# Kernel tuning notes

Measured on AMD Instinct MI355X. Metric: run time of the kernel, lower is better.

The kernel has to match this reference:

```python
import jax, jax.numpy as jnp
import numpy as np

BS, L = 4096, 20
NF, EF, TF = 128, 128, 128
DM = 3 * NF + EF + TF          # 640: attention model dim
DIN = DM - TF                  # 512: GRU input dim
NHEAD = 2
NNODES, NEDGES = 100000, 500000
ODE_STEPS = 8


def setup_inputs() -> dict:
    key = jax.random.key(0)
    ks = jax.random.split(key, 32)
    p = lambda i, shape, s: jax.random.normal(ks[i], shape, dtype=jnp.float32) * s
    return {
        'nids': jax.random.randint(ks[0], (BS,), 1, NNODES),
        'ts': jax.random.uniform(ks[1], (BS,), dtype=jnp.float32),
        'hist_nids': jax.random.randint(ks[2], (BS, L), 0, NNODES),
        'anonymized_ids': jax.random.randint(ks[3], (BS, L), 0, L + 1),
        'hist_eids': jax.random.randint(ks[4], (BS, L), 0, NEDGES),
        'hist_ts': jnp.sort(jax.random.uniform(ks[5], (BS, L), dtype=jnp.float32), axis=1),
        'hist_dirs': jax.random.randint(ks[6], (BS, L), 0, 2),
        'node_feat': p(7, (NNODES, NF), 0.1),
        'edge_feat': p(8, (NEDGES, EF), 0.1),
        'anony_emb': p(9, (L + 1, NF), 0.1),
        'time_w': p(10, (TF,), 1.0),
        'time_b': p(11, (TF,), 1.0),
        'in_proj_w': p(12, (3 * DM, DM), 0.02),
        'in_proj_b': jnp.zeros((3 * DM,), jnp.float32),
        'out_proj_w': p(13, (DM, DM), 0.02),
        'out_proj_b': jnp.zeros((DM,), jnp.float32),
        'outfn_w': p(14, (NF, DM), 0.02),
        'outfn_b': jnp.zeros((NF,), jnp.float32),
        'attn_wq': p(15, (NF, NF), 0.05),
        'attn_wk': p(16, (NF + EF + TF, NF), 0.05),
        'attn_wv': p(17, (NF + EF + TF, NF), 0.05),
        'merge_w': p(18, (2 * NF, NF), 0.05),
        'merge_b': jnp.zeros((NF,), jnp.float32),
        'gru_w_ih': p(19, (3 * NF, DIN), 0.05),
        'gru_w_hh': p(20, (3 * NF, NF), 0.05),
        'gru_b_ih': jnp.zeros((3 * NF,), jnp.float32),
        'gru_b_hh': jnp.zeros((3 * NF,), jnp.float32),
        'ode_w': p(21, (NF, NF), 0.05),
        'ode_b': jnp.zeros((NF,), jnp.float32),
        'tnode_w': p(22, (NF,), 1.0),
        'tnode_b': p(23, (NF,), 1.0),
    }


def reference(nids, ts, hist_nids, anonymized_ids, hist_eids, hist_ts, hist_dirs,
              node_feat, edge_feat, anony_emb, time_w, time_b,
              in_proj_w, in_proj_b, out_proj_w, out_proj_b, outfn_w, outfn_b,
              attn_wq, attn_wk, attn_wv, merge_w, merge_b,
              gru_w_ih, gru_w_hh, gru_b_ih, gru_b_hh,
              ode_w, ode_b, tnode_w, tnode_b):
    bs, hl = hist_nids.shape
    mask = (hist_nids == 0)
    mask = mask.at[:, -1].set(False)
    invalid_rows = jnp.all(mask, axis=1, keepdims=True)  # [bs,1]

    r_nids = jnp.broadcast_to(nids[:, None], (bs, hl))
    src_nids = r_nids * hist_dirs + hist_nids * (1 - hist_dirs)
    dst_nids = r_nids * (1 - hist_dirs) + hist_nids * hist_dirs

    src_vals = node_feat[src_nids]                 # [bs,L,NF] gather
    dst_vals = node_feat[dst_nids]                 # [bs,L,NF] gather
    edge_vals = edge_feat[hist_eids]               # [bs,L,EF] gather
    anony_vals = anony_emb[anonymized_ids]         # [bs,L,NF] gather
    dt = hist_ts[:, -1:] - hist_ts                 # [bs,L]
    ts_vals = jnp.cos(dt[..., None] * time_w + time_b)  # [bs,L,TF] TimeEncode

    full_vals = jnp.concatenate([src_vals, dst_vals, anony_vals, edge_vals, ts_vals], axis=2)
    last_event_feat = full_vals[:, -1, :DIN]
    full_vals = full_vals.at[:, -1, :DIN].set(0.0)

    # --- self MHA over history (nn.MultiheadAttention with key_padding_mask) ---
    qkv = full_vals @ in_proj_w.T + in_proj_b      # [bs,L,3*DM]
    q, k, v = jnp.split(qkv, 3, axis=-1)
    dh = DM // NHEAD
    rs = lambda x: x.reshape(bs, hl, NHEAD, dh)
    scores = jnp.einsum('blhd,bmhd->bhlm', rs(q), rs(k)) / np.sqrt(dh)
    scores = jnp.where(mask[:, None, None, :], -1e9, scores)
    attn = jax.nn.softmax(scores, axis=-1)
    ctx = jnp.einsum('bhlm,bmhd->blhd', attn, rs(v)).reshape(bs, hl, DM)
    mha_out = ctx @ out_proj_w.T + out_proj_b

    # --- temporal graph attention embedding (GraphAttnEmbedding stand-in) ---
    qn = mha_out[:, -1] @ outfn_w.T + outfn_b      # [bs,NF]
    nb = jnp.concatenate([node_feat[hist_nids], edge_vals, ts_vals], axis=2)  # [bs,L,NF+EF+TF]
    qh = qn @ attn_wq                              # [bs,NF]
    kh = nb @ attn_wk                              # [bs,L,NF]
    vh = nb @ attn_wv                              # [bs,L,NF]
    sc = jnp.einsum('bd,bld->bl', qh, kh) / np.sqrt(NF)
    sc = jnp.where(mask, -1e9, sc)
    a = jax.nn.softmax(sc, axis=-1)
    ctx2 = jnp.einsum('bl,bld->bd', a, vh)
    h_prev_left = jnp.tanh(jnp.concatenate([ctx2, node_feat[nids]], axis=1) @ merge_w + merge_b)

    # --- GRUCell jump update ---
    gi = last_event_feat @ gru_w_ih.T + gru_b_ih
    gh = h_prev_left @ gru_w_hh.T + gru_b_hh
    ir, iz, inn = jnp.split(gi, 3, axis=-1)
    hr, hz, hn = jnp.split(gh, 3, axis=-1)
    r = jax.nn.sigmoid(ir + hr)
    zg = jax.nn.sigmoid(iz + hz)
    n = jnp.tanh(inn + r * hn)
    h_prev_right = (1.0 - zg) * n + zg * h_prev_left

    # --- neural ODE transform (RK4 over s in [0,1]) ---
    t0 = hist_ts[:, -2:-1]                         # prev_prev_ts [bs,1]
    t1 = hist_ts[:, -1:]                           # prev_ts      [bs,1]
    ratio = t1 - t0                                # (end-start)=1.0

    def f(s, z):
        t = s * ratio + t0                         # [bs,1]
        te = jnp.cos(t * tnode_w + tnode_b)        # [bs,NF]
        return jnp.tanh((z + te) @ ode_w.T + ode_b) * ratio

    ds = 1.0 / ODE_STEPS

    def step(z, s):
        k1 = f(s, z)
        k2 = f(s + 0.5 * ds, z + 0.5 * ds * k1)
        k3 = f(s + 0.5 * ds, z + 0.5 * ds * k2)
        k4 = f(s + ds, z + ds * k3)
        return z + (ds / 6.0) * (k1 + 2 * k2 + 2 * k3 + k4), None

    h_left, _ = jax.lax.scan(step, h_prev_right, jnp.arange(ODE_STEPS, dtype=jnp.float32) * ds)

    h_left = jnp.where(invalid_rows, 0.0, h_left)
    h_right = jnp.where(invalid_rows, 0.0, h_prev_right)
    return h_left, h_right, hist_ts[:, -1]
```

## Files before the change

kernel.cpp:

```cpp
#include <hip/hip_runtime.h>
#include <math.h>

#define BSZ 4096
#define HL  20
#define NF  128
#define DM  640
#define DIN 512
#define DH  320

static __device__ __forceinline__ float sigmoidf_(float x){ return 1.f/(1.f+expf(-x)); }
static __device__ __forceinline__ unsigned short f2b_(float v){
    return (unsigned short)((__float_as_uint(v) + 0x8000u) >> 16);
}
static __device__ __forceinline__ float b2f_(unsigned short u){
    return __uint_as_float(((unsigned int)u) << 16);
}

__global__ void k_comb(const float* __restrict__ outfn_w,
                       const float* __restrict__ out_proj_w,
                       float* __restrict__ combT)
{
    int jc = blockIdx.x, jq = threadIdx.x;
    float acc = 0.f;
    for (int e = 0; e < DM; ++e)
        acc += outfn_w[jq*DM + e] * out_proj_w[e*DM + jc];
    combT[jc*NF + jq] = acc;
}

__global__ void k_zz(const float* __restrict__ in_proj_w,
                     const float* __restrict__ combT,
                     float* __restrict__ ZZ)
{
    int ef = blockIdx.x;
    int h = ef / DM, e = ef - h*DM;
    int jq = threadIdx.x;
    const float* wv = in_proj_w + (2*DM + h*DH)*DM + e;
    const float* cb = combT + (h*DH)*NF + jq;
    float acc = 0.f;
    for (int dd = 0; dd < DH; ++dd)
        acc += wv[dd*DM] * cb[dd*NF];
    ZZ[ef*NF + jq] = acc;
}

__global__ void k_qbias(const float* __restrict__ outfn_b,
                        const float* __restrict__ out_proj_b,
                        const float* __restrict__ outfn_w,
                        const float* __restrict__ in_proj_b,
                        const float* __restrict__ combT,
                        float* __restrict__ qb)
{
    int jq = threadIdx.x;
    float acc = outfn_b[jq];
    for (int e = 0; e < DM; ++e)  acc += out_proj_b[e] * outfn_w[jq*DM + e];
    for (int jc = 0; jc < DM; ++jc) acc += in_proj_b[2*DM + jc] * combT[jc*NF + jq];
    qb[jq] = acc;
}

__global__ void k_transpose(const float* __restrict__ gih,
                            const float* __restrict__ ghh,
                            float* __restrict__ giT,
                            float* __restrict__ ghT)
{
    int i = blockIdx.x*blockDim.x + threadIdx.x;
    if (i < DIN*3*NF) {
        int d = i / (3*NF), j = i - d*(3*NF);
        giT[i] = gih[j*DIN + d];
    } else {
        int i2 = i - DIN*3*NF;
        int d = i2 / (3*NF), j = i2 - d*(3*NF);
        ghT[i2] = ghh[j*NF + d];
    }
}

__global__ void k_qc(const float* __restrict__ time_b,
                     const float* __restrict__ in_proj_w,
                     const float* __restrict__ in_proj_b,
                     float* __restrict__ qcv)
{
    __shared__ float tsr[NF];
    int tid = threadIdx.x;
    tsr[tid] = cosf(time_b[tid]);
    __syncthreads();
    int j = blockIdx.x*128 + tid;
    const float* wr = in_proj_w + j*DM + DIN;
    float acc = in_proj_b[j];
    for (int d = 0; d < NF; ++d) acc += tsr[d]*wr[d];
    qcv[j] = acc;
}

__global__ void k_cc(const float* __restrict__ qcv,
                     const float* __restrict__ in_proj_b,
                     float* __restrict__ cc)
{
    int wave = threadIdx.x >> 6, lane = threadIdx.x & 63;
    float acc = 0.f;
    for (int j = lane; j < DH; j += 64)
        acc += qcv[wave*DH + j] * in_proj_b[DM + wave*DH + j];
    for (int off = 32; off > 0; off >>= 1) acc += __shfl_down(acc, off);
    if (lane == 0) cc[wave] = acc;
}

__global__ void k_u(const float* __restrict__ qcv,
                    const float* __restrict__ in_proj_w,
                    float* __restrict__ u)
{
    int d = blockIdx.x*64 + threadIdx.x;
    int h = d / DM, dd = d - h*DM;
    const float* base = in_proj_w + (DM + h*DH)*DM + dd;
    const float* q = qcv + h*DH;
    float acc = 0.f;
    for (int j = 0; j < DH; ++j) acc += q[j]*base[j*DM];
    u[d] = acc;
}

__global__ __launch_bounds__(256) void k_attn1(
    const int* __restrict__ nids, const int* __restrict__ hist_nids,
    const int* __restrict__ aidsp, const int* __restrict__ eidsp,
    const float* __restrict__ hist_ts, const int* __restrict__ dirsp,
    const float* __restrict__ node_feat, const float* __restrict__ edge_feat,
    const float* __restrict__ anony_emb,
    const float* __restrict__ time_w, const float* __restrict__ time_b,
    const float* __restrict__ u, const float* __restrict__ cc,
    float* __restrict__ wbuf, float* __restrict__ lef)
{
    int b = blockIdx.x, tid = threadIdx.x;
    int wave = tid >> 6, lane = tid & 63;
    __shared__ unsigned short zh[HL][DM];
    __shared__ float ul[2*DM];
    __shared__ float sc[2][HL];
    __shared__ float aw[2][HL];
    __shared__ int   shn[HL], sdir[HL], said[HL], seid[HL];
    __shared__ float sts[HL];

    if (tid < HL) {
        shn[tid]  = hist_nids[b*HL+tid];
        sdir[tid] = dirsp[b*HL+tid];
        said[tid] = aidsp[b*HL+tid];
        seid[tid] = eidsp[b*HL+tid];
        sts[tid]  = hist_ts[b*HL+tid];
    }
    for (int i = tid; i < 2*DM; i += 256) ul[i] = u[i];
    float twA = time_w[lane],    tbA = time_b[lane];
    float twB = time_w[64+lane], tbB = time_b[64+lane];
    __syncthreads();

    float ulr0[10], ulr1[10];
    #pragma unroll
    for (int s = 0; s < 10; ++s) {
        ulr0[s] = ul[s*64 + lane];
        ulr1[s] = ul[DM + s*64 + lane];
    }

    int rnid = nids[b];
    float tlast = sts[HL-1];

    int srcv[5], dstv[5], aidv[5], eidv[5];
    float dtv[5];
    #pragma unroll
    for (int r = 0; r < 5; ++r) {
        int l = wave + 4*r;
        int hn = shn[l], dir = sdir[l];
        srcv[r] = dir ? rnid : hn;
        dstv[r] = dir ? hn : rnid;
        aidv[r] = said[l];
        eidv[r] = eidv[r] = seid[l];
        dtv[r]  = tlast - sts[l];
    }
    float zr[5][10];
    #pragma unroll
    for (int r = 0; r < 5; ++r) {
        zr[r][0] = node_feat[srcv[r]*NF + lane];
        zr[r][1] = node_feat[srcv[r]*NF + 64 + lane];
        zr[r][2] = node_feat[dstv[r]*NF + lane];
        zr[r][3] = node_feat[dstv[r]*NF + 64 + lane];
        zr[r][4] = anony_emb[aidv[r]*NF + lane];
        zr[r][5] = anony_emb[aidv[r]*NF + 64 + lane];
        zr[r][6] = edge_feat[eidv[r]*NF + lane];
        zr[r][7] = edge_feat[eidv[r]*NF + 64 + lane];
        zr[r][8] = cosf(dtv[r]*twA + tbA);
        zr[r][9] = cosf(dtv[r]*twB + tbB);
    }
    float c0 = cc[0], c1 = cc[1];
    #pragma unroll
    for (int r = 0; r < 5; ++r) {
        int l = wave + 4*r;
        if (l == HL-1) {
            #pragma unroll
            for (int s = 0; s < 8; ++s) {
                lef[b*DIN + s*64 + lane] = zr[r][s];
                zr[r][s] = 0.f;
            }
        }
        float d0 = 0.f, d1 = 0.f;
        #pragma unroll
        for (int s = 0; s < 10; ++s) {
            float v = zr[r][s];
            d0 += ulr0[s]*v;
            d1 += ulr1[s]*v;
            zh[l][s*64 + lane] = f2b_(v);
        }
        for (int off = 32; off > 0; off >>= 1) {
            d0 += __shfl_down(d0, off);
            d1 += __shfl_down(d1, off);
        }
        if (lane == 0) {
            bool msk = (shn[l] == 0) && (l != HL-1);
            sc[0][l] = msk ? -1.0e9f : (d0 + c0)*0.05590169943749474f;
            sc[1][l] = msk ? -1.0e9f : (d1 + c1)*0.05590169943749474f;
        }
    }
    __syncthreads();
    if (tid < 2) {
        float mx = -3.0e38f;
        for (int m = 0; m < HL; ++m) mx = fmaxf(mx, sc[tid][m]);
        float sum = 0.f;
        for (int m = 0; m < HL; ++m) { float e = expf(sc[tid][m]-mx); aw[tid][m] = e; sum += e; }
        float inv = 1.f/sum;
        for (int m = 0; m < HL; ++m) aw[tid][m] *= inv;
    }
    __syncthreads();
    #pragma unroll
    for (int i = tid; i < 2*DM; i += 256) {
        int h = i / DM, d = i - h*DM;
        float acc = 0.f;
        #pragma unroll
        for (int m = 0; m < HL; ++m) acc += aw[h][m]*b2f_(zh[m][d]);
        wbuf[b*2*DM + i] = acc;
    }
}

__global__ __launch_bounds__(256) void k_gemm_qn(const float* __restrict__ A,
                                                 const float* __restrict__ BT,
                                                 const float* __restrict__ bias,
                                                 float* __restrict__ C)
{
    constexpr int K = 2*DM;
    __shared__ float As[8*K];
    int r0 = blockIdx.x*8, tid = threadIdx.x;
    for (int i = tid; i < 8*K; i += 256) As[i] = A[r0*K + i];
    __syncthreads();
    int j = tid & (NF-1), rh = tid >> 7;
    const float* bp = BT + j;
    const float* ap = As + rh*4*K;
    float acc0=0.f, acc1=0.f, acc2=0.f, acc3=0.f;
    for (int d = 0; d < K; ++d) {
        float bv = bp[d*NF];
        acc0 += ap[d]*bv;
        acc1 += ap[K + d]*bv;
        acc2 += ap[2*K + d]*bv;
        acc3 += ap[3*K + d]*bv;
    }
    float bsv = bias[j];
    int rb = r0 + rh*4;
    C[(rb+0)*NF + j] = acc0 + bsv;
    C[(rb+1)*NF + j] = acc1 + bsv;
    C[(rb+2)*NF + j] = acc2 + bsv;
    C[(rb+3)*NF + j] = acc3 + bsv;
}

__global__ __launch_bounds__(256) void k_gemm_gi(const float* __restrict__ A,
                                                 const float* __restrict__ BT,
                                                 const float* __restrict__ bias,
                                                 float* __restrict__ C)
{
    constexpr int K = DIN;
    constexpr int N = 3*NF;
    __shared__ float As[8*K];
    int r0 = blockIdx.x*8, tid = threadIdx.x;
    for (int i = tid; i < 8*K; i += 256) As[i] = A[r0*K + i];
    __syncthreads();
    int j0 = tid, j1 = tid + 256;
    bool has1 = (j1 < N);
    float a0[8] = {0,0,0,0,0,0,0,0};
    float a1[8] = {0,0,0,0,0,0,0,0};
    for (int d = 0; d < K; ++d) {
        float b0 = BT[d*N + j0];
        float b1 = 0.f;
        if (has1) b1 = BT[d*N + j1];
        #pragma unroll
        for (int r = 0; r < 8; ++r) {
            float av = As[r*K + d];
            a0[r] += av*b0;
            a1[r] += av*b1;
        }
    }
    float bs0 = bias[j0];
    for (int r = 0; r < 8; ++r) C[(r0+r)*N + j0] = a0[r] + bs0;
    if (has1) {
        float bs1 = bias[j1];
        for (int r = 0; r < 8; ++r) C[(r0+r)*N + j1] = a1[r] + bs1;
    }
}

__global__ __launch_bounds__(128) void k_attn2(
    const int* __restrict__ nids, const int* __restrict__ hist_nids,
    const int* __restrict__ eidsp, const float* __restrict__ hist_ts,
    const float* __restrict__ node_feat, const float* __restrict__ edge_feat,
    const float* __restrict__ time_w, const float* __restrict__ time_b,
    const float* __restrict__ attn_wq, const float* __restrict__ attn_wk,
    const float* __restrict__ attn_wv,
    const float* __restrict__ merge_w, const float* __restrict__ merge_b,
    const float* __restrict__ qn, const float* __restrict__ gi,
    const float* __restrict__ ghT, const float* __restrict__ gru_b_hh,
    float* __restrict__ hpr_out, float* __restrict__ out)
{
    int b = blockIdx.x, tid = threadIdx.x;
    __shared__ float qns[NF], qh[NF], p[3*NF], nbar[3*NF];
    __shared__ float scl[HL], al[HL];
    __shared__ float ctx2[NF], hpl[NF], nfn[NF];
    __shared__ int   shn[HL], seid[HL];
    __shared__ float sts[HL];

    if (tid < HL) {
        shn[tid]  = hist_nids[b*HL+tid];
        seid[tid] = eidsp[b*HL+tid];
        sts[tid]  = hist_ts[b*HL+tid];
    }
    qns[tid] = qn[b*NF + tid];
    nfn[tid] = node_feat[nids[b]*NF + tid];
    __syncthreads();

    float tlast = sts[HL-1];
    {
        float acc = 0.f;
        for (int d = 0; d < NF; ++d) acc += qns[d]*attn_wq[d*NF + tid];
        qh[tid] = acc;
    }
    __syncthreads();
    for (int dd = tid; dd < 3*NF; dd += NF) {
        const float4* row4 = (const float4*)(attn_wk + dd*NF);
        float acc = 0.f;
        #pragma unroll
        for (int q4 = 0; q4 < NF/4; ++q4) {
            float4 w4 = row4[q4];
            acc += w4.x*qh[4*q4] + w4.y*qh[4*q4+1] + w4.z*qh[4*q4+2] + w4.w*qh[4*q4+3];
        }
        p[dd] = acc;
    }
    __syncthreads();
    int wave = tid >> 6, lane = tid & 63;
    for (int l = wave; l < HL; l += 2) {
        int hn = shn[l], eid = seid[l];
        float dt = tlast - sts[l];
        float acc = 0.f;
        #pragma unroll
        for (int kk = 0; kk < 6; ++kk) {
            int d = lane + 64*kk;
            float v;
            if (d < NF)            v = node_feat[hn*NF + d];
            else if (d < 2*NF)     v = edge_feat[eid*NF + (d-NF)];
            else { int dd = d-2*NF; v = cosf(dt*time_w[dd] + time_b[dd]); }
            acc += p[d]*v;
        }
        for (int off = 32; off > 0; off >>= 1) acc += __shfl_down(acc, off);
        if (lane == 0) {
            bool msk = (hn == 0) && (l != HL-1);
            scl[l] = msk ? -1.0e9f : acc*0.08838834764831845f;
        }
    }
    __syncthreads();
    if (tid == 0) {
        float mx = -3.0e38f;
        for (int m = 0; m < HL; ++m) mx = fmaxf(mx, scl[m]);
        float sum = 0.f;
        for (int m = 0; m < HL; ++m) { float e = expf(scl[m]-mx); al[m] = e; sum += e; }
        float inv = 1.f/sum;
        for (int m = 0; m < HL; ++m) al[m] *= inv;
    }
    __syncthreads();
    {
        float twj = time_w[tid], tbj = time_b[tid];
        float an = 0.f, ae = 0.f, at = 0.f;
        #pragma unroll
        for (int l = 0; l < HL; ++l) {
            float a = al[l];
            an += a*node_feat[shn[l]*NF + tid];
            ae += a*edge_feat[seid[l]*NF + tid];
            at += a*cosf((tlast - sts[l])*twj + tbj);
        }
        nbar[tid]       = an;
        nbar[tid+NF]    = ae;
        nbar[tid+2*NF]  = at;
    }
    __syncthreads();
    {
        float acc = 0.f;
        for (int d = 0; d < 3*NF; ++d) acc += nbar[d]*attn_wv[d*NF + tid];
        ctx2[tid] = acc;
    }
    __syncthreads();
    {
        float acc = merge_b[tid];
        for (int d = 0; d < NF; ++d) acc += ctx2[d]*merge_w[d*NF + tid];
        for (int d = 0; d < NF; ++d) acc += nfn[d]*merge_w[(NF+d)*NF + tid];
        hpl[tid] = tanhf(acc);
    }
    __syncthreads();
    float ghv[3];
    #pragma unroll
    for (int s = 0; s < 3; ++s) {
        int jj = s*NF + tid;
        float acc = gru_b_hh[jj];
        for (int d = 0; d < NF; ++d) acc += hpl[d]*ghT[d*3*NF + jj];
        ghv[s] = acc;
    }
    float gi0 = gi[b*3*NF + tid];
    float gi1 = gi[b*3*NF + NF + tid];
    float gi2 = gi[b*3*NF + 2*NF + tid];
    float r_ = sigmoidf_(gi0 + ghv[0]);
    float z_ = sigmoidf_(gi1 + ghv[1]);
    float n_ = tanhf(gi2 + r_*ghv[2]);
    float hpr = (1.f - z_)*n_ + z_*hpl[tid];
    out[BSZ*NF + b*NF + tid] = hpr;
    hpr_out[b*NF + tid] = hpr;
    if (tid == 0) out[2*BSZ*NF + b] = tlast;
}

static __device__ __forceinline__ void ode_eval2(
    const float yin0, const float yin1, const float4* __restrict__ wr, float obj,
    const float rat0, const float rat1, float* __restrict__ yb, int j, int g,
    float* k0, float* k1)
{
    __syncthreads();
    yb[(2*g+0)*NF + j] = yin0;
    yb[(2*g+1)*NF + j] = yin1;
    __syncthreads();
    const float4* yA4 = (const float4*)(yb + (2*g+0)*NF);
    const float4* yB4 = (const float4*)(yb + (2*g+1)*NF);
    float a0 = obj, a1 = obj, b0 = 0.f, b1 = 0.f;
    #pragma unroll
    for (int q = 0; q < 32; q += 2) {
        float4 w0 = wr[q],   w1 = wr[q+1];
        float4 ya0 = yA4[q], yc0 = yB4[q];
        float4 ya1 = yA4[q+1], yc1 = yB4[q+1];
        a0 += w0.x*ya0.x + w0.y*ya0.y + w0.z*ya0.z + w0.w*ya0.w;
        a1 += w0.x*yc0.x + w0.y*yc0.y + w0.z*yc0.z + w0.w*yc0.w;
        b0 += w1.x*ya1.x + w1.y*ya1.y + w1.z*ya1.z + w1.w*ya1.w;
        b1 += w1.x*yc1.x + w1.y*yc1.y + w1.z*yc1.z + w1.w*yc1.w;
    }
    *k0 = tanhf(a0 + b0)*rat0;
    *k1 = tanhf(a1 + b1)*rat1;
}

__global__ __launch_bounds__(256) void k_ode(
    const float* __restrict__ hpr, const float* __restrict__ hist_ts,
    const float* __restrict__ ode_w, const float* __restrict__ ode_b,
    const float* __restrict__ tnode_w, const float* __restrict__ tnode_b,
    float* __restrict__ out)
{
    __shared__ float yb[4*NF];
    int tid = threadIdx.x;
    int j = tid & (NF-1), g = tid >> 7;
    int b0 = blockIdx.x*4 + g*2;

    float4 wr[32];
    const float4* owr = (const float4*)(ode_w + j*NF);
    #pragma unroll
    for (int i = 0; i < 32; ++i) wr[i] = owr[i];
    float twj = tnode_w[j], tbj = tnode_b[j], obj = ode_b[j];

    float z0, z1, t00, t01, rat0, rat1;
    {
        float t1a = hist_ts[(b0+0)*HL + (HL-1)];
        float t1b = hist_ts[(b0+1)*HL + (HL-1)];
        t00 = hist_ts[(b0+0)*HL + (HL-2)];
        t01 = hist_ts[(b0+1)*HL + (HL-2)];
        rat0 = t1a - t00; rat1 = t1b - t01;
        z0 = hpr[(b0+0)*NF + j];
        z1 = hpr[(b0+1)*NF + j];
    }

    const float dss = 0.125f;
    #pragma unroll 1
    for (int stp = 0; stp < 8; ++stp) {
        float s0 = stp*dss;
        float teA0 = cosf((s0*rat0 + t00)*twj + tbj);
        float teA1 = cosf((s0*rat1 + t01)*twj + tbj);
        float teB0 = cosf(((s0 + 0.0625f)*rat0 + t00)*twj + tbj);
        float teB1 = cosf(((s0 + 0.0625f)*rat1 + t01)*twj + tbj);
        float teC0 = cosf(((s0 + 0.125f)*rat0 + t00)*twj + tbj);
        float teC1 = cosf(((s0 + 0.125f)*rat1 + t01)*twj + tbj);
        float k10, k11, k20, k21, k30, k31, k40, k41;
        ode_eval2(z0 + teA0,               z1 + teA1,               wr, obj, rat0, rat1, yb, j, g, &k10, &k11);
        ode_eval2(z0 + 0.0625f*k10 + teB0, z1 + 0.0625f*k11 + teB1, wr, obj, rat0, rat1, yb, j, g, &k20, &k21);
        ode_eval2(z0 + 0.0625f*k20 + teB0, z1 + 0.0625f*k21 + teB1, wr, obj, rat0, rat1, yb, j, g, &k30, &k31);
        ode_eval2(z0 + 0.125f*k30 + teC0,  z1 + 0.125f*k31 + teC1,  wr, obj, rat0, rat1, yb, j, g, &k40, &k41);
        z0 += (0.125f/6.f)*(k10 + 2.f*k20 + 2.f*k30 + k40);
        z1 += (0.125f/6.f)*(k11 + 2.f*k21 + 2.f*k31 + k41);
    }
    out[(b0+0)*NF + j] = z0;
    out[(b0+1)*NF + j] = z1;
}

extern "C" void kernel_launch(void* const* d_in, const int* in_sizes, int n_in,
                              void* d_out, int out_size, void* d_ws, size_t ws_size,
                              hipStream_t stream)
{
    (void)in_sizes; (void)n_in; (void)out_size; (void)ws_size;
    const int*   nids      = (const int*)d_in[0];
    const int*   hist_nids = (const int*)d_in[2];
    const int*   aids      = (const int*)d_in[3];
    const int*   eids      = (const int*)d_in[4];
    const float* hist_ts   = (const float*)d_in[5];
    const int*   dirs      = (const int*)d_in[6];
    const float* node_feat = (const float*)d_in[7];
    const float* edge_feat = (const float*)d_in[8];
    const float* anony_emb = (const float*)d_in[9];
    const float* time_w    = (const float*)d_in[10];
    const float* time_b    = (const float*)d_in[11];
    const float* in_proj_w = (const float*)d_in[12];
    const float* in_proj_b = (const float*)d_in[13];
    const float* out_proj_w= (const float*)d_in[14];
    const float* out_proj_b= (const float*)d_in[15];
    const float* outfn_w   = (const float*)d_in[16];
    const float* outfn_b   = (const float*)d_in[17];
    const float* attn_wq   = (const float*)d_in[18];
    const float* attn_wk   = (const float*)d_in[19];
    const float* attn_wv   = (const float*)d_in[20];
    const float* merge_w   = (const float*)d_in[21];
    const float* merge_b   = (const float*)d_in[22];
    const float* gru_w_ih  = (const float*)d_in[23];
    const float* gru_w_hh  = (const float*)d_in[24];
    const float* gru_b_ih  = (const float*)d_in[25];
    const float* gru_b_hh  = (const float*)d_in[26];
    const float* ode_w     = (const float*)d_in[27];
    const float* ode_b     = (const float*)d_in[28];
    const float* tnode_w   = (const float*)d_in[29];
    const float* tnode_b   = (const float*)d_in[30];
    float* out = (float*)d_out;

    float* ws    = (float*)d_ws;
    float* qc    = ws;
    float* cc    = ws + 640;
    float* u     = ws + 768;
    float* wbuf  = ws + 2048;
    float* lef   = wbuf + BSZ*2*DM;
    float* qn    = lef + BSZ*DIN;
    float* gi    = qn + BSZ*NF;
    float* combT = gi + BSZ*3*NF;
    float* ZZ    = combT + DM*NF;
    float* qb    = ZZ + 2*DM*NF;
    float* giT   = qb + NF;
    float* ghT   = giT + DIN*3*NF;
    float* hpr   = wbuf;

    k_comb<<<DM, NF, 0, stream>>>(outfn_w, out_proj_w, combT);
    k_zz<<<2*DM, NF, 0, stream>>>(in_proj_w, combT, ZZ);
    k_qbias<<<1, NF, 0, stream>>>(outfn_b, out_proj_b, outfn_w, in_proj_b, combT, qb);
    k_transpose<<<960, 256, 0, stream>>>(gru_w_ih, gru_w_hh, giT, ghT);
    k_qc<<<5, 128, 0, stream>>>(time_b, in_proj_w, in_proj_b, qc);
    k_cc<<<1, 128, 0, stream>>>(qc, in_proj_b, cc);
    k_u<<<HL, 64, 0, stream>>>(qc, in_proj_w, u);

    k_attn1<<<BSZ, 256, 0, stream>>>(nids, hist_nids, aids, eids, hist_ts, dirs,
                                     node_feat, edge_feat, anony_emb,
                                     time_w, time_b, u, cc, wbuf, lef);
    k_gemm_qn<<<BSZ/8, 256, 0, stream>>>(wbuf, ZZ, qb, qn);
    k_gemm_gi<<<BSZ/8, 256, 0, stream>>>(lef, giT, gru_b_ih, gi);
    k_attn2<<<BSZ, 128, 0, stream>>>(nids, hist_nids, eids, hist_ts,
                                     node_feat, edge_feat, time_w, time_b,
                                     attn_wq, attn_wk, attn_wv, merge_w, merge_b,
                                     qn, gi, ghT, gru_b_hh, hpr, out);
    k_ode<<<BSZ/4, 256, 0, stream>>>(hpr, hist_ts, ode_w, ode_b,
                                     tnode_w, tnode_b, out);
}
```

Baseline: 1.126 ms.

## Split ODE weight rows across thread pairs and double-buffer shared state

The ODE kernel now gives each output column to two threads that each hold half a weight row (16 float4 instead of 32), combining partial dot products with a lane shuffle. This cuts register pressure so more waves can be resident (launch bounds request 4 blocks). It also alternates between two shared buffers so each eval needs one barrier instead of two, reuses the end-of-step cosine as the next step's start value, and launches twice as many blocks with two rows each. The costs are duplicated cosine and state work in both threads of a pair, plus an extra shuffle per eval.

After: 1.097 ms. 1.03x faster.

```diff
diff --git a/kernel.cpp b/kernel.cpp
--- a/kernel.cpp
+++ b/kernel.cpp
@@ -416,47 +416,51 @@
     if (tid == 0) out[2*BSZ*NF + b] = tlast;
 }
 
-static __device__ __forceinline__ void ode_eval2(
-    const float yin0, const float yin1, const float4* __restrict__ wr, float obj,
-    const float rat0, const float rat1, float* __restrict__ yb, int j, int g,
-    float* k0, float* k1)
-{
-    __syncthreads();
-    yb[(2*g+0)*NF + j] = yin0;
-    yb[(2*g+1)*NF + j] = yin1;
-    __syncthreads();
-    const float4* yA4 = (const float4*)(yb + (2*g+0)*NF);
-    const float4* yB4 = (const float4*)(yb + (2*g+1)*NF);
-    float a0 = obj, a1 = obj, b0 = 0.f, b1 = 0.f;
-    #pragma unroll
-    for (int q = 0; q < 32; q += 2) {
-        float4 w0 = wr[q],   w1 = wr[q+1];
-        float4 ya0 = yA4[q], yc0 = yB4[q];
-        float4 ya1 = yA4[q+1], yc1 = yB4[q+1];
-        a0 += w0.x*ya0.x + w0.y*ya0.y + w0.z*ya0.z + w0.w*ya0.w;
-        a1 += w0.x*yc0.x + w0.y*yc0.y + w0.z*yc0.z + w0.w*yc0.w;
-        b0 += w1.x*ya1.x + w1.y*ya1.y + w1.z*ya1.z + w1.w*ya1.w;
-        b1 += w1.x*yc1.x + w1.y*yc1.y + w1.z*yc1.z + w1.w*yc1.w;
-    }
-    *k0 = tanhf(a0 + b0)*rat0;
-    *k1 = tanhf(a1 + b1)*rat1;
-}
-
-__global__ __launch_bounds__(256) void k_ode(
+static __device__ __forceinline__ void ode_eval_pair(
+    float y0, float y1,
+    const float4* __restrict__ wr,
+    float ob, float rat0, float rat1,
+    float* __restrict__ zrow,
+    int j, int h, float* k0, float* k1)
+{
+    if (h == 0) zrow[j]      = y0;
+    else        zrow[NF + j] = y1;
+    __syncthreads();
+    const float4* zA = (const float4*)(zrow + h*64);
+    const float4* zB = (const float4*)(zrow + NF + h*64);
+    float a0 = 0.f, b0 = 0.f, a1 = 0.f, b1 = 0.f;
+    #pragma unroll
+    for (int q = 0; q < 16; q += 2) {
+        float4 w0 = wr[q],  w1 = wr[q+1];
+        float4 xA0 = zA[q], xA1 = zA[q+1];
+        float4 xB0 = zB[q], xB1 = zB[q+1];
+        a0 += w0.x*xA0.x + w0.y*xA0.y + w0.z*xA0.z + w0.w*xA0.w;
+        b0 += w1.x*xA1.x + w1.y*xA1.y + w1.z*xA1.z + w1.w*xA1.w;
+        a1 += w0.x*xB0.x + w0.y*xB0.y + w0.z*xB0.z + w0.w*xB0.w;
+        b1 += w1.x*xB1.x + w1.y*xB1.y + w1.z*xB1.z + w1.w*xB1.w;
+    }
+    float s0 = a0 + b0, s1 = a1 + b1;
+    s0 += __shfl_xor(s0, 1);
+    s1 += __shfl_xor(s1, 1);
+    *k0 = tanhf(s0 + ob)*rat0;
+    *k1 = tanhf(s1 + ob)*rat1;
+}
+
+__global__ __launch_bounds__(256, 4) void k_ode(
     const float* __restrict__ hpr, const float* __restrict__ hist_ts,
     const float* __restrict__ ode_w, const float* __restrict__ ode_b,
     const float* __restrict__ tnode_w, const float* __restrict__ tnode_b,
     float* __restrict__ out)
 {
-    __shared__ float yb[4*NF];
+    __shared__ float zb[2][2][NF];
     int tid = threadIdx.x;
-    int j = tid & (NF-1), g = tid >> 7;
-    int b0 = blockIdx.x*4 + g*2;
-
-    float4 wr[32];
-    const float4* owr = (const float4*)(ode_w + j*NF);
-    #pragma unroll
-    for (int i = 0; i < 32; ++i) wr[i] = owr[i];
+    int j = tid >> 1, h = tid & 1;
+    int b0 = blockIdx.x*2;
+
+    float4 wr[16];
+    const float4* wp = (const float4*)(ode_w + j*NF + h*64);
+    #pragma unroll
+    for (int i = 0; i < 16; ++i) wr[i] = wp[i];
     float twj = tnode_w[j], tbj = tnode_b[j], obj = ode_b[j];
 
     float z0, z1, t00, t01, rat0, rat1;
@@ -470,26 +474,28 @@
         z1 = hpr[(b0+1)*NF + j];
     }
 
-    const float dss = 0.125f;
+    float teA0 = cosf(t00*twj + tbj);
+    float teA1 = cosf(t01*twj + tbj);
     #pragma unroll 1
     for (int stp = 0; stp < 8; ++stp) {
-        float s0 = stp*dss;
-        float teA0 = cosf((s0*rat0 + t00)*twj + tbj);
-        float teA1 = cosf((s0*rat1 + t01)*twj + tbj);
+        float s0 = stp*0.125f;
         float teB0 = cosf(((s0 + 0.0625f)*rat0 + t00)*twj + tbj);
         float teB1 = cosf(((s0 + 0.0625f)*rat1 + t01)*twj + tbj);
         float teC0 = cosf(((s0 + 0.125f)*rat0 + t00)*twj + tbj);
         float teC1 = cosf(((s0 + 0.125f)*rat1 + t01)*twj + tbj);
         float k10, k11, k20, k21, k30, k31, k40, k41;
-        ode_eval2(z0 + teA0,               z1 + teA1,               wr, obj, rat0, rat1, yb, j, g, &k10, &k11);
-        ode_eval2(z0 + 0.0625f*k10 + teB0, z1 + 0.0625f*k11 + teB1, wr, obj, rat0, rat1, yb, j, g, &k20, &k21);
-        ode_eval2(z0 + 0.0625f*k20 + teB0, z1 + 0.0625f*k21 + teB1, wr, obj, rat0, rat1, yb, j, g, &k30, &k31);
-        ode_eval2(z0 + 0.125f*k30 + teC0,  z1 + 0.125f*k31 + teC1,  wr, obj, rat0, rat1, yb, j, g, &k40, &k41);
+        ode_eval_pair(z0 + teA0,               z1 + teA1,               wr, obj, rat0, rat1, &zb[0][0][0], j, h, &k10, &k11);
+        ode_eval_pair(z0 + 0.0625f*k10 + teB0, z1 + 0.0625f*k11 + teB1, wr, obj, rat0, rat1, &zb[1][0][0], j, h, &k20, &k21);
+        ode_eval_pair(z0 + 0.0625f*k20 + teB0, z1 + 0.0625f*k21 + teB1, wr, obj, rat0, rat1, &zb[0][0][0], j, h, &k30, &k31);
+        ode_eval_pair(z0 + 0.125f*k30 + teC0,  z1 + 0.125f*k31 + teC1,  wr, obj, rat0, rat1, &zb[1][0][0], j, h, &k40, &k41);
         z0 += (0.125f/6.f)*(k10 + 2.f*k20 + 2.f*k30 + k40);
         z1 += (0.125f/6.f)*(k11 + 2.f*k21 + 2.f*k31 + k41);
-    }
-    out[(b0+0)*NF + j] = z0;
-    out[(b0+1)*NF + j] = z1;
+        teA0 = teC0; teA1 = teC1;
+    }
+    if (h == 0) {
+        out[(b0+0)*NF + j] = z0;
+        out[(b0+1)*NF + j] = z1;
+    }
 }
 
 extern "C" void kernel_launch(void* const* d_in, const int* in_sizes, int n_in,
@@ -561,6 +567,6 @@
                                      node_feat, edge_feat, time_w, time_b,
                                      attn_wq, attn_wk, attn_wv, merge_w, merge_b,
                                      qn, gi, ghT, gru_b_hh, hpr, out);
-    k_ode<<<BSZ/4, 256, 0, stream>>>(hpr, hist_ts, ode_w, ode_b,
+    k_ode<<<BSZ/2, 256, 0, stream>>>(hpr, hist_ts, ode_w, ode_b,
                                      tnode_w, tnode_b, out);
 }
```
